# Performance work log

Measured on AMD Instinct MI355X. Metric: run time of the kernel, lower is better.

The kernel has to match this reference:

```python
import jax, jax.numpy as jnp
import numpy as np

N_NODES = 100000
N_EDGES = 1600000
IN_F = 64
HIDDEN = 128
HIDDEN2 = HIDDEN // 2
N_CLASSES = 10


def setup_inputs() -> dict:
    key = jax.random.key(0)
    ks = jax.random.split(key, 8)
    x = jax.random.normal(ks[0], (N_NODES, IN_F), dtype=jnp.float32)
    edge_index = jax.random.randint(ks[1], (2, N_EDGES), 0, N_NODES, dtype=jnp.int64 if jax.config.jax_enable_x64 else jnp.int32)
    # Linear params (PyTorch nn.Linear: y = x @ W.T + b); store as [in, out] for einsum-free matmul
    def lin(k, fi, fo):
        bound = 1.0 / np.sqrt(fi)
        kw, kb = jax.random.split(k)
        W = jax.random.uniform(kw, (fi, fo), minval=-bound, maxval=bound, dtype=jnp.float32)
        b = jax.random.uniform(kb, (fo,), minval=-bound, maxval=bound, dtype=jnp.float32)
        return W, b
    W1, b1 = lin(ks[2], IN_F, HIDDEN)
    W2, b2 = lin(ks[3], HIDDEN, HIDDEN2)
    W3, b3 = lin(ks[4], HIDDEN2, N_CLASSES)
    return {"x": x, "edge_index": edge_index, "n_nodes": N_NODES,
            "W1": W1, "b1": b1, "W2": W2, "b2": b2, "W3": W3, "b3": b3}


def gcn_layer(x, row, col, n_nodes, W, b):
    # gather source features, scatter-add into destination nodes
    agg = jax.ops.segment_sum(x[row], col, num_segments=n_nodes)  # [N, F]
    deg = jax.ops.segment_sum(jnp.ones_like(col, dtype=x.dtype), col, num_segments=n_nodes)
    deg = jnp.maximum(deg, 1.0)
    return (agg / deg[:, None]) @ W + b


def reference(x, edge_index, n_nodes, W1, b1, W2, b2, W3, b3):
    row, col = edge_index[0], edge_index[1]
    h = jax.nn.relu(gcn_layer(x, row, col, n_nodes, W1, b1))
    # dropout is identity in eval mode
    h = jax.nn.relu(gcn_layer(h, row, col, n_nodes, W2, b2))
    return h @ W3 + b3
```

## Files before the change

### kernel.cpp

```cpp
#include <hip/hip_runtime.h>

#define N_NODES 100000
#define N_EDGES 1600000
#define IN_F 64
#define HID 128
#define HID2 64
#define NCLS 10

#define NRANGE 8
#define RANGE_NODES ((N_NODES + NRANGE - 1) / NRANGE)
#define EBLK 128
#define ECHUNK (N_EDGES / EBLK)

#define SEG 64

typedef __attribute__((ext_vector_type(8))) short bfrag;
typedef __attribute__((ext_vector_type(4))) float f32x4;

__device__ __forceinline__ unsigned short bf_rne(float f) {
  unsigned int u = __float_as_uint(f);
  u += 0x7fffu + ((u >> 16) & 1u);
  return (unsigned short)(u >> 16);
}

__global__ __launch_bounds__(256) void cast_k(const float* __restrict__ x,
                                              unsigned short* __restrict__ xb) {
  int i = blockIdx.x * blockDim.x + threadIdx.x;
  const float4* xf4 = (const float4*)x;
  float4 a = xf4[2 * i];
  float4 b = xf4[2 * i + 1];
  ushort4 o0, o1;
  o0.x = bf_rne(a.x); o0.y = bf_rne(a.y); o0.z = bf_rne(a.z); o0.w = bf_rne(a.w);
  o1.x = bf_rne(b.x); o1.y = bf_rne(b.y); o1.z = bf_rne(b.z); o1.w = bf_rne(b.w);
  ushort4* ob = (ushort4*)xb;
  ob[2 * i] = o0;
  ob[2 * i + 1] = o1;
}

__global__ __launch_bounds__(256) void wtrans_k(const float* __restrict__ W1,
                                                const float* __restrict__ W2,
                                                unsigned short* __restrict__ W1t,
                                                unsigned short* __restrict__ W2t) {
  int i = blockIdx.x * 256 + threadIdx.x;
  if (i < IN_F * HID) {
    int j = i >> 6, k = i & 63;
    W1t[i] = bf_rne(W1[k * HID + j]);
  } else {
    int i2 = i - IN_F * HID;
    int j = i2 >> 7, k = i2 & 127;
    W2t[i2] = bf_rne(W2[k * HID2 + j]);
  }
}

__global__ __launch_bounds__(256) void curs_init_k(int* __restrict__ cursors) {
  int n = blockIdx.x * blockDim.x + threadIdx.x;
  if (n < N_NODES) cursors[n] = n * SEG;
}

__global__ __launch_bounds__(256) void fill2_k(const int* __restrict__ row,
                                               const int* __restrict__ col,
                                               int* __restrict__ cursors,
                                               int* __restrict__ csr_src) {
  int r = blockIdx.x & (NRANGE - 1);
  int j = blockIdx.x >> 3;
  int lo = r * RANGE_NODES, hi = lo + RANGE_NODES;
  int e0 = j * ECHUNK, e1 = e0 + ECHUNK;
  for (int e = e0 + threadIdx.x; e < e1; e += 256) {
    int dst = col[e];
    int src = row[e];
    if (dst >= lo && dst < hi) {
      int pos = atomicAdd(&cursors[dst], 1);
      csr_src[pos] = src;
    }
  }
}

__device__ __forceinline__ float4 gather_bf16(const uint2* __restrict__ vb,
                                              const int* __restrict__ csr,
                                              int s, int e2, int padc,
                                              int eg, int fc) {
  float ax = 0.f, ay = 0.f, az = 0.f, aw = 0.f;
  const int4* csr4 = (const int4*)csr;
#define ACCUM(w)                                                    \
  {                                                                 \
    ax += __uint_as_float((w).x << 16);                             \
    ay += __uint_as_float((w).x & 0xffff0000u);                     \
    az += __uint_as_float((w).y << 16);                             \
    aw += __uint_as_float((w).y & 0xffff0000u);                     \
  }
  int p = s;
  for (; p + 32 <= e2; p += 32) {
    int4 iA = csr4[(p >> 2) + eg];
    int4 iB = csr4[((p + 16) >> 2) + eg];
    uint2 a0 = vb[(size_t)iA.x * 16 + fc];
    uint2 a1 = vb[(size_t)iA.y * 16 + fc];
    uint2 a2 = vb[(size_t)iA.z * 16 + fc];
    uint2 a3 = vb[(size_t)iA.w * 16 + fc];
    uint2 b0 = vb[(size_t)iB.x * 16 + fc];
    uint2 b1 = vb[(size_t)iB.y * 16 + fc];
    uint2 b2 = vb[(size_t)iB.z * 16 + fc];
    uint2 b3 = vb[(size_t)iB.w * 16 + fc];
    ACCUM(a0) ACCUM(a1) ACCUM(a2) ACCUM(a3)
    ACCUM(b0) ACCUM(b1) ACCUM(b2) ACCUM(b3)
  }
  if (p < e2) {
    int4 iA = csr4[(p >> 2) + eg];
    uint2 a0 = vb[(size_t)iA.x * 16 + fc];
    uint2 a1 = vb[(size_t)iA.y * 16 + fc];
    uint2 a2 = vb[(size_t)iA.z * 16 + fc];
    uint2 a3 = vb[(size_t)iA.w * 16 + fc];
    ACCUM(a0) ACCUM(a1) ACCUM(a2) ACCUM(a3)
  }
#undef ACCUM
  ax += __shfl_xor(ax, 16); ay += __shfl_xor(ay, 16);
  az += __shfl_xor(az, 16); aw += __shfl_xor(aw, 16);
  ax += __shfl_xor(ax, 32); ay += __shfl_xor(ay, 32);
  az += __shfl_xor(az, 32); aw += __shfl_xor(aw, 32);
  uint2 z = vb[fc];
  float pc = (float)padc;
  ax -= pc * __uint_as_float(z.x << 16);
  ay -= pc * __uint_as_float(z.x & 0xffff0000u);
  az -= pc * __uint_as_float(z.y << 16);
  aw -= pc * __uint_as_float(z.y & 0xffff0000u);
  return make_float4(ax, ay, az, aw);
}

#define NB1 32
#define XS_S 72
#define HS_S 136
#define W1_S 72
#define W2_S 136
__global__ __launch_bounds__(512) void gmm1_k(
    const unsigned short* __restrict__ xb, const int* __restrict__ cursors,
    const int* __restrict__ csr_src, const unsigned short* __restrict__ W1t,
    const float* __restrict__ b1, const unsigned short* __restrict__ W2t,
    unsigned short* __restrict__ g) {
  __shared__ unsigned short W1l[HID * W1_S];
  __shared__ unsigned short W2l[HID2 * W2_S];
  __shared__ unsigned short xsb[NB1 * XS_S];
  __shared__ unsigned short hsb[NB1 * HS_S];
  __shared__ float b1l[HID];
  int t = threadIdx.x;
  {
    const uint2* s1 = (const uint2*)W1t;
    for (int i = t; i < HID * IN_F / 4; i += 512) {
      int j = i >> 4, k4 = i & 15;
      *(uint2*)&W1l[j * W1_S + k4 * 4] = s1[i];
    }
    const uint2* s2 = (const uint2*)W2t;
    for (int i = t; i < HID2 * HID / 4; i += 512) {
      int j = i >> 5, k4 = i & 31;
      *(uint2*)&W2l[j * W2_S + k4 * 4] = s2[i];
    }
    if (t < HID) b1l[t] = b1[t];
  }
  int node0 = blockIdx.x * NB1;
  int wave = t >> 6;
  int lane = t & 63;
  int eg = lane >> 4;
  int fc = lane & 15;
  {
    const uint2* xv = (const uint2*)xb;
    for (int i = 0; i < 4; i++) {
      int ln = wave * 4 + i;
      int n = node0 + ln;
      int s = n * SEG;
      int d = cursors[n] - s;
      int dp = (d + 15) & ~15;
      float4 a = gather_bf16(xv, csr_src, s, s + dp, dp - d, eg, fc);
      float inv = 1.0f / (d < 1 ? 1.0f : (float)d);
      if (eg == 0) {
        ushort4 o;
        o.x = bf_rne(a.x * inv); o.y = bf_rne(a.y * inv);
        o.z = bf_rne(a.z * inv); o.w = bf_rne(a.w * inv);
        *(ushort4*)&xsb[ln * XS_S + fc * 4] = o;
      }
    }
  }
  __syncthreads();
  int lr = lane & 15;
  int kb = lane >> 4;
  {
    int c = wave;
#pragma unroll
    for (int m = 0; m < 2; m++) {
      f32x4 acc = {0.f, 0.f, 0.f, 0.f};
#pragma unroll
      for (int s = 0; s < 2; s++) {
        bfrag af = *(const bfrag*)&xsb[(m * 16 + lr) * XS_S + s * 32 + kb * 8];
        bfrag bf = *(const bfrag*)&W1l[(c * 16 + lr) * W1_S + s * 32 + kb * 8];
        acc = __builtin_amdgcn_mfma_f32_16x16x32_bf16(af, bf, acc, 0, 0, 0);
      }
      int col = c * 16 + lr;
      float bb = b1l[col];
#pragma unroll
      for (int q = 0; q < 4; q++) {
        int r = m * 16 + kb * 4 + q;
        float v = acc[q] + bb;
        hsb[r * HS_S + col] = bf_rne(v > 0.0f ? v : 0.0f);
      }
    }
  }
  __syncthreads();
  {
    int m = wave >> 2, c = wave & 3;
    f32x4 acc = {0.f, 0.f, 0.f, 0.f};
#pragma unroll
    for (int s = 0; s < 4; s++) {
      bfrag af = *(const bfrag*)&hsb[(m * 16 + lr) * HS_S + s * 32 + kb * 8];
      bfrag bf = *(const bfrag*)&W2l[(c * 16 + lr) * W2_S + s * 32 + kb * 8];
      acc = __builtin_amdgcn_mfma_f32_16x16x32_bf16(af, bf, acc, 0, 0, 0);
    }
    int col = c * 16 + lr;
#pragma unroll
    for (int q = 0; q < 4; q++) {
      int r = m * 16 + kb * 4 + q;
      g[(size_t)(node0 + r) * HID2 + col] = bf_rne(acc[q]);
    }
  }
}

#define NBH 32
__global__ __launch_bounds__(512) void ghead_k(
    const unsigned short* __restrict__ g, const int* __restrict__ cursors,
    const int* __restrict__ csr_src, const float* __restrict__ b2,
    const float* __restrict__ W3, const float* __restrict__ b3,
    float* __restrict__ out) {
  __shared__ float W3l[HID2 * NCLS];
  __shared__ float hs[NBH][HID2 + 4];
  int t = threadIdx.x;
  for (int i = t; i < HID2 * NCLS; i += 512) W3l[i] = W3[i];
  int node0 = blockIdx.x * NBH;
  int lane = t & 63;
  int wave = t >> 6;
  int eg = lane >> 4;
  int fc = lane & 15;
  const uint2* gv = (const uint2*)g;
  const float4* b2f4 = (const float4*)b2;
  for (int i = 0; i < 4; i++) {
    int ln = wave * 4 + i;
    int n = node0 + ln;
    int s = n * SEG;
    int d = cursors[n] - s;
    int dp = (d + 15) & ~15;
    float4 a = gather_bf16(gv, csr_src, s, s + dp, dp - d, eg, fc);
    float inv = 1.0f / (d < 1 ? 1.0f : (float)d);
    if (eg == 0) {
      float4 bb = b2f4[fc];
      float4 v;
      v.x = a.x * inv + bb.x; v.y = a.y * inv + bb.y;
      v.z = a.z * inv + bb.z; v.w = a.w * inv + bb.w;
      v.x = v.x > 0.0f ? v.x : 0.0f;
      v.y = v.y > 0.0f ? v.y : 0.0f;
      v.z = v.z > 0.0f ? v.z : 0.0f;
      v.w = v.w > 0.0f ? v.w : 0.0f;
      *(float4*)&hs[ln][fc * 4] = v;
    }
  }
  __syncthreads();
  if (t < NBH * NCLS) {
    int n = t / NCLS;
    int c = t - n * NCLS;
    float a = b3[c];
    for (int k = 0; k < HID2; k++) a += hs[n][k] * W3l[k * NCLS + c];
    out[(size_t)(node0 + n) * NCLS + c] = a;
  }
}

extern "C" void kernel_launch(void* const* d_in, const int* in_sizes, int n_in,
                              void* d_out, int out_size, void* d_ws, size_t ws_size,
                              hipStream_t stream) {
  const float* x  = (const float*)d_in[0];
  const int*   ei = (const int*)d_in[1];
  const int*   row = ei;
  const int*   col = ei + N_EDGES;
  const float* W1 = (const float*)d_in[3];
  const float* b1 = (const float*)d_in[4];
  const float* W2 = (const float*)d_in[5];
  const float* b2 = (const float*)d_in[6];
  const float* W3 = (const float*)d_in[7];
  const float* b3 = (const float*)d_in[8];
  float* out = (float*)d_out;

  char* ws = (char*)d_ws;
  int*            cursors = (int*)ws;
  unsigned short* W1t     = (unsigned short*)(ws + (512 << 10));
  unsigned short* W2t     = (unsigned short*)(ws + (544 << 10));
  int*            csr_src = (int*)(ws + (1 << 20));
  unsigned short* xb      = (unsigned short*)(ws + (28 << 20));
  unsigned short* g       = (unsigned short*)(ws + (42 << 20));

  hipMemsetAsync(csr_src, 0, (size_t)N_NODES * SEG * sizeof(int), stream);
  curs_init_k<<<(N_NODES + 255) / 256, 256, 0, stream>>>(cursors);
  wtrans_k<<<(IN_F * HID + HID * HID2) / 256, 256, 0, stream>>>(W1, W2, W1t, W2t);
  cast_k<<<N_NODES * IN_F / 8 / 256, 256, 0, stream>>>(x, xb);
  fill2_k<<<NRANGE * EBLK, 256, 0, stream>>>(row, col, cursors, csr_src);

  gmm1_k<<<N_NODES / NB1, 512, 0, stream>>>(xb, cursors, csr_src, W1t, b1, W2t, g);

  ghead_k<<<N_NODES / NBH, 512, 0, stream>>>(g, cursors, csr_src, b2, W3, b3, out);
}
```

Baseline: 184.7 us.

## Replace range-filtered CSR fill with two-pass destination-range binning

The old fill kernel had every block re-read a chunk of all edges once per destination range (8x redundant reads of row/col) and kept only matching ones. The new version first bins edges into per-range pair buffers using shared-memory histograms and one global atomic per range per block, then a second kernel scatters each bin into the per-node CSR segments. This removes the redundant edge reads and keeps the per-node atomics localized to one range at a time, at the cost of an extra kernel and an intermediate pair buffer write and read. CAP assumes no range exceeds 210000 edges, which holds for uniformly random inputs.

Result: slower. 200.6 us (+8.6%).

```diff
diff --git a/kernel.cpp b/kernel.cpp
--- a/kernel.cpp
+++ b/kernel.cpp
@@ -9,10 +9,12 @@
 
 #define NRANGE 8
 #define RANGE_NODES ((N_NODES + NRANGE - 1) / NRANGE)
-#define EBLK 128
-#define ECHUNK (N_EDGES / EBLK)
 
 #define SEG 64
+
+#define CAP 210000
+#define EBA 6250
+#define PBCHUNK ((CAP + 63) / 64)
 
 typedef __attribute__((ext_vector_type(8))) short bfrag;
 typedef __attribute__((ext_vector_type(4))) float f32x4;
@@ -57,21 +59,51 @@
   if (n < N_NODES) cursors[n] = n * SEG;
 }
 
-__global__ __launch_bounds__(256) void fill2_k(const int* __restrict__ row,
-                                               const int* __restrict__ col,
-                                               int* __restrict__ cursors,
-                                               int* __restrict__ csr_src) {
+__global__ __launch_bounds__(256) void binA_k(const int* __restrict__ row,
+                                              const int* __restrict__ col,
+                                              int* __restrict__ bcnt,
+                                              int2* __restrict__ pairs) {
+  __shared__ int hcnt[NRANGE];
+  __shared__ int hbase[NRANGE];
+  int t = threadIdx.x;
+  if (t < NRANGE) hcnt[t] = 0;
+  __syncthreads();
+  int e0 = blockIdx.x * EBA;
+  int e1 = e0 + EBA;
+  for (int e = e0 + t; e < e1; e += 256) {
+    int b = col[e] / RANGE_NODES;
+    atomicAdd(&hcnt[b], 1);
+  }
+  __syncthreads();
+  if (t < NRANGE) {
+    hbase[t] = atomicAdd(&bcnt[t], hcnt[t]);
+    hcnt[t] = 0;
+  }
+  __syncthreads();
+  for (int e = e0 + t; e < e1; e += 256) {
+    int dst = col[e];
+    int src = row[e];
+    int b = dst / RANGE_NODES;
+    int pos = hbase[b] + atomicAdd(&hcnt[b], 1);
+    pairs[(size_t)b * CAP + pos] = make_int2(dst, src);
+  }
+}
+
+__global__ __launch_bounds__(256) void binB_k(const int2* __restrict__ pairs,
+                                              const int* __restrict__ bcnt,
+                                              int* __restrict__ cursors,
+                                              int* __restrict__ csr_src) {
   int r = blockIdx.x & (NRANGE - 1);
   int j = blockIdx.x >> 3;
-  int lo = r * RANGE_NODES, hi = lo + RANGE_NODES;
-  int e0 = j * ECHUNK, e1 = e0 + ECHUNK;
-  for (int e = e0 + threadIdx.x; e < e1; e += 256) {
-    int dst = col[e];
-    int src = row[e];
-    if (dst >= lo && dst < hi) {
-      int pos = atomicAdd(&cursors[dst], 1);
-      csr_src[pos] = src;
-    }
+  int cnt = bcnt[r];
+  int i0 = j * PBCHUNK;
+  int i1 = i0 + PBCHUNK;
+  if (i1 > cnt) i1 = cnt;
+  const int2* bp = pairs + (size_t)r * CAP;
+  for (int i = i0 + threadIdx.x; i < i1; i += 256) {
+    int2 p = bp[i];
+    int pos = atomicAdd(&cursors[p.x], 1);
+    csr_src[pos] = p.y;
   }
 }
 
@@ -284,17 +316,21 @@
 
   char* ws = (char*)d_ws;
   int*            cursors = (int*)ws;
-  unsigned short* W1t     = (unsigned short*)(ws + (512 << 10));
-  unsigned short* W2t     = (unsigned short*)(ws + (544 << 10));
+  int*            bcnt    = (int*)(ws + (512 << 10));
+  unsigned short* W1t     = (unsigned short*)(ws + (520 << 10));
+  unsigned short* W2t     = (unsigned short*)(ws + (552 << 10));
   int*            csr_src = (int*)(ws + (1 << 20));
-  unsigned short* xb      = (unsigned short*)(ws + (28 << 20));
-  unsigned short* g       = (unsigned short*)(ws + (42 << 20));
+  int2*           pairs   = (int2*)(ws + (28 << 20));
+  unsigned short* xb      = (unsigned short*)(ws + (42 << 20));
+  unsigned short* g       = (unsigned short*)(ws + (56 << 20));
 
   hipMemsetAsync(csr_src, 0, (size_t)N_NODES * SEG * sizeof(int), stream);
+  hipMemsetAsync(bcnt, 0, NRANGE * sizeof(int), stream);
   curs_init_k<<<(N_NODES + 255) / 256, 256, 0, stream>>>(cursors);
   wtrans_k<<<(IN_F * HID + HID * HID2) / 256, 256, 0, stream>>>(W1, W2, W1t, W2t);
   cast_k<<<N_NODES * IN_F / 8 / 256, 256, 0, stream>>>(x, xb);
-  fill2_k<<<NRANGE * EBLK, 256, 0, stream>>>(row, col, cursors, csr_src);
+  binA_k<<<N_EDGES / EBA, 256, 0, stream>>>(row, col, bcnt, pairs);
+  binB_k<<<NRANGE * 64, 256, 0, stream>>>(pairs, bcnt, cursors, csr_src);
 
   gmm1_k<<<N_NODES / NB1, 512, 0, stream>>>(xb, cursors, csr_src, W1t, b1, W2t, g);
 
```
